# Kernel optimization log

Hardware: AMD Instinct MI355X
Metric: run time of the kernel (lower is better)

The kernel has to match this reference:

```python
import jax, jax.numpy as jnp
import numpy as np

EPS = 1e-5
NUM_GROUPS = 16


def _deform_conv(x, offset, mask, weight):
    """Modulated deformable conv v2, 3x3, stride 1, pad 1, no bias.
    x: [B,C,H,W], offset: [B,18,H,W] (y,x interleaved per kernel point),
    mask: [B,9,H,W], weight: [O,C,3,3].
    """
    B, C, H, W = x.shape
    O = weight.shape[0]
    K = 9
    off = offset.reshape(B, K, 2, H, W)
    dy, dx = off[:, :, 0], off[:, :, 1]  # [B,K,H,W]
    # base sampling grid: output pixel + kernel tap offset (pad=1 -> taps -1..1)
    ky, kx = jnp.meshgrid(jnp.arange(3), jnp.arange(3), indexing='ij')
    ky = (ky.reshape(K) - 1).astype(x.dtype)
    kx = (kx.reshape(K) - 1).astype(x.dtype)
    iy = jnp.arange(H, dtype=x.dtype)[:, None]
    ix = jnp.arange(W, dtype=x.dtype)[None, :]
    py = iy[None, None] + ky[None, :, None, None] + dy  # [B,K,H,W]
    px = ix[None, None] + kx[None, :, None, None] + dx

    y0 = jnp.floor(py)
    x0 = jnp.floor(px)
    wy = py - y0  # grad flows to offsets via these weights
    wx = px - x0

    xf = x.reshape(B, C, H * W)

    def gather(yc, xc, w):
        # yc,xc,w: [B,K,H,W] float; returns weighted samples [B,C,K,H,W]
        valid = (yc >= 0) & (yc <= H - 1) & (xc >= 0) & (xc <= W - 1)
        yi = jnp.clip(yc, 0, H - 1).astype(jnp.int32)
        xi = jnp.clip(xc, 0, W - 1).astype(jnp.int32)
        idx = (yi * W + xi).reshape(B, K * H * W)
        g = jax.vmap(lambda xb, ib: xb[:, ib])(xf, idx)  # [B,C,K*H*W]
        g = g.reshape(B, C, K, H, W)
        wv = (w * valid.astype(x.dtype))[:, None]  # [B,1,K,H,W]
        return g * wv

    val = gather(y0, x0, (1 - wy) * (1 - wx))
    val = val + gather(y0, x0 + 1, (1 - wy) * wx)
    val = val + gather(y0 + 1, x0, wy * (1 - wx))
    val = val + gather(y0 + 1, x0 + 1, wy * wx)

    val = val * mask[:, None]  # modulation: [B,C,K,H,W] * [B,1,K,H,W]
    w = weight.reshape(O, C, K)
    return jnp.einsum('bckhw,ock->bohw', val, w)


def _group_norm(y, gamma, beta):
    B, O, H, W = y.shape
    g = y.reshape(B, NUM_GROUPS, O // NUM_GROUPS, H, W)
    mean = g.mean(axis=(2, 3, 4), keepdims=True)
    var = ((g - mean) ** 2).mean(axis=(2, 3, 4), keepdims=True)
    g = (g - mean) * jax.lax.rsqrt(var + EPS)
    y = g.reshape(B, O, H, W)
    return y * gamma[None, :, None, None] + beta[None, :, None, None]


def setup_inputs() -> dict:
    key = jax.random.key(0)
    k1, k2, k3, k4 = jax.random.split(key, 4)
    B, C, O, H, W = 8, 256, 256, 64, 64
    x = jax.random.normal(k1, (B, C, H, W), jnp.float32)
    offset = jax.random.normal(k2, (B, 18, H, W), jnp.float32)
    mask = jax.random.uniform(k3, (B, 9, H, W), jnp.float32)
    weight = jax.random.normal(k4, (O, C, 3, 3), jnp.float32) * 0.02
    gamma = jnp.ones((O,), jnp.float32)
    beta = jnp.zeros((O,), jnp.float32)
    return {"x": x, "offset": offset, "mask": mask, "weight": weight,
            "gamma": gamma, "beta": beta}


def reference(x, offset, mask, weight, gamma, beta):
    y = _deform_conv(x, offset, mask, weight)
    return _group_norm(y, gamma, beta)
```

## Files before the change

kernel.cpp:

```cpp
#include <hip/hip_runtime.h>
#include <hip/hip_fp16.h>
#include <math.h>

#define BB 8
#define CC 256
#define OO 256
#define HH 64
#define WW 64
#define KK 9
#define HWSZ 4096
#define CKSZ 2304
#define NG 16
#define OPG 16
#define EPSV 1e-5f

typedef _Float16 f16;
typedef f16 f16x8 __attribute__((ext_vector_type(8)));
typedef float f32x4 __attribute__((ext_vector_type(4)));

#define XH_ELEMS ((size_t)BB*HWSZ*CC)
#define WF_ELEMS ((size_t)OO*CKSZ)
#define CV_ELEMS ((size_t)BB*OO*HWSZ)
#define NSTRIP 32

__global__ __launch_bounds__(256) void x_transpose_k(
    const float* __restrict__ x, __half* __restrict__ xh)
{
  int blk = blockIdx.x;
  int b = blk >> 8; int rem = blk & 255;
  int c0 = (rem >> 6) * 64; int hw0 = (rem & 63) * 64;
  __shared__ float st[64][65];
  int t = threadIdx.x;
  #pragma unroll
  for (int i = 0; i < 16; ++i) {
    int idx = t + i*256; int c = idx >> 6, w = idx & 63;
    st[c][w] = x[((size_t)(b*CC + c0 + c))*HWSZ + hw0 + w];
  }
  __syncthreads();
  #pragma unroll
  for (int i = 0; i < 8; ++i) {
    int idx = t + i*256; int r = idx >> 5, cp = idx & 31;
    __half2 v = __floats2half2_rn(st[cp*2][r], st[cp*2+1][r]);
    *(__half2*)&xh[((size_t)(b*HWSZ) + hw0 + r)*CC + c0 + cp*2] = v;
  }
}

__global__ __launch_bounds__(256) void w_frag_k(
    const float* __restrict__ w, __half* __restrict__ wf)
{
  int i = blockIdx.x*256 + threadIdx.x;
  int e = i & 7, lane = (i >> 3) & 63, mi = (i >> 9) & 3;
  int ks = (i >> 11) & 1, wm = (i >> 12) & 3, cc = i >> 14;
  int k = cc >> 2, c0i = cc & 3;
  int o = wm*64 + mi*16 + (lane & 15);
  int c = c0i*64 + ks*32 + (lane >> 4)*8 + e;
  wf[i] = __float2half(w[(o*CC + c)*KK + k]);
}

template<int F16OUT>
__global__ __launch_bounds__(512, 2) void dcn_mfma_k(
    const float* __restrict__ off, const float* __restrict__ msk,
    const __half* __restrict__ xh, const __half* __restrict__ wf,
    float* __restrict__ out32, __half* __restrict__ conv16,
    float* __restrict__ psum)
{
  __shared__ __half sVl[4][128*64];

  const int t = threadIdx.x;
  const int b = blockIdx.x & 7;
  const int strip = blockIdx.x >> 3;
  const int h0 = strip * 2;

  const int lane = t & 63, wid = t >> 6;
  const int lr = lane & 15, lh = lane >> 4;
  const int gp = t >> 2, gq = t & 3;

  auto load_A = [&](int cc, f16x8 a[2][2]) {
    #pragma unroll
    for (int ks = 0; ks < 2; ++ks)
      #pragma unroll
      for (int mi = 0; mi < 2; ++mi) {
        int omi = wid*2 + mi;
        const __half* ap = wf + (size_t)(cc*4 + (omi >> 2))*4096
                              + (size_t)(ks*4 + (omi & 3))*512 + lane*8;
        a[ks][mi] = *(const f16x8*)ap;
      }
  };

  f16x8 aregA[2][2], aregB[2][2];
  load_A(0, aregA);
  load_A(1, aregB);

  f32x4 acc[2][8];
  #pragma unroll
  for (int mi = 0; mi < 2; ++mi)
    #pragma unroll
    for (int ni = 0; ni < 8; ++ni) acc[mi][ni] = (f32x4){0.f,0.f,0.f,0.f};

  const char* xbase = (const char*)xh + (size_t)b * (HWSZ*CC*2);

  uint toff[4]; __half2 twv[4];
  auto compute_taps = [&](int k) {
    int h = h0 + (gp >> 6), w = gp & 63;
    float dy = off[(((b*18) + 2*k    )*HH + h)*WW + w];
    float dx = off[(((b*18) + 2*k + 1)*HH + h)*WW + w];
    float m  = msk[(((b*KK) + k)*HH + h)*WW + w];
    float py = (float)(h + (k/3) - 1) + dy;
    float px = (float)(w + (k%3) - 1) + dx;
    float y0f = floorf(py), x0f = floorf(px);
    float wy = py - y0f, wx = px - x0f;
    int y0 = (int)y0f, x0 = (int)x0f;
    #pragma unroll
    for (int tap = 0; tap < 4; ++tap) {
      int yy = y0 + (tap >> 1), xx = x0 + (tap & 1);
      bool v = (yy >= 0) & (yy < HH) & (xx >= 0) & (xx < WW);
      float bw = ((tap >> 1) ? wy : 1.f - wy) * ((tap & 1) ? wx : 1.f - wx);
      float wgt = v ? bw * m : 0.f;
      int cy = min(max(yy, 0), HH-1), cx = min(max(xx, 0), WW-1);
      toff[tap] = (uint)((cy*WW + cx) * (CC*2));
      twv[tap]  = __float2half2_rn(wgt);
    }
  };
  int tk = 0;
  compute_taps(0);

  auto combine_write = [&](uint4 r0, uint4 r1, uint4 r2, uint4 r3,
                           int oct, __half* dst) {
    const __half2* t0 = (const __half2*)&r0; const __half2* t1 = (const __half2*)&r1;
    const __half2* t2 = (const __half2*)&r2; const __half2* t3 = (const __half2*)&r3;
    __half2 o_[4];
    #pragma unroll
    for (int r = 0; r < 4; ++r)
      o_[r] = __hfma2(twv[0], t0[r], __hfma2(twv[1], t1[r],
              __hfma2(twv[2], t2[r], __hmul2(twv[3], t3[r]))));
    *(uint4*)&dst[gp*64 + ((oct ^ (gp & 7)) << 3)] = *(uint4*)o_;
  };

  auto gather_chunk = [&](int cc, __half* dst) {
    int kn = cc >> 2, c0n = (cc & 3) << 6;
    if (kn != tk) { compute_taps(kn); tk = kn; }
    const char* cb = xbase + (size_t)(c0n*2) + gq*16;
    uint4 a0 = *(const uint4*)(cb + toff[0]);
    uint4 a1 = *(const uint4*)(cb + toff[1]);
    uint4 a2 = *(const uint4*)(cb + toff[2]);
    uint4 a3 = *(const uint4*)(cb + toff[3]);
    uint4 b0 = *(const uint4*)(cb + toff[0] + 64);
    uint4 b1 = *(const uint4*)(cb + toff[1] + 64);
    uint4 b2 = *(const uint4*)(cb + toff[2] + 64);
    uint4 b3 = *(const uint4*)(cb + toff[3] + 64);
    combine_write(a0, a1, a2, a3, gq,     dst);
    combine_write(b0, b1, b2, b3, gq + 4, dst);
  };

  gather_chunk(0, sVl[0]);
  gather_chunk(1, sVl[1]);

  auto do_half = [&](int ccm, int ccf, f16x8 aCur[2][2]) {
    bool pf = (ccf < 36);
    int kn = ccf >> 2, c0n = (ccf & 3) << 6;
    uint4 ga0, ga1, ga2, ga3, gb0, gb1, gb2, gb3;
    if (pf) {
      if (kn != tk) { compute_taps(kn); tk = kn; }
      const char* cb = xbase + (size_t)(c0n*2) + gq*16;
      ga0 = *(const uint4*)(cb + toff[0]);
      ga1 = *(const uint4*)(cb + toff[1]);
      ga2 = *(const uint4*)(cb + toff[2]);
      ga3 = *(const uint4*)(cb + toff[3]);
      gb0 = *(const uint4*)(cb + toff[0] + 64);
      gb1 = *(const uint4*)(cb + toff[1] + 64);
      gb2 = *(const uint4*)(cb + toff[2] + 64);
      gb3 = *(const uint4*)(cb + toff[3] + 64);
    }

    const __half* vb = sVl[ccm & 3];
    #pragma unroll
    for (int ks = 0; ks < 2; ++ks) {
      f16x8 brg[8];
      #pragma unroll
      for (int ni = 0; ni < 8; ++ni) {
        int r = ni*16 + lr;
        brg[ni] = *(const f16x8*)&vb[r*64 + (((ks*4 + lh) ^ (r & 7)) << 3)];
      }
      #pragma unroll
      for (int mi = 0; mi < 2; ++mi)
        #pragma unroll
        for (int ni = 0; ni < 8; ++ni)
          acc[mi][ni] = __builtin_amdgcn_mfma_f32_16x16x32_f16(
              aCur[ks][mi], brg[ni], acc[mi][ni], 0, 0, 0);
    }

    if (pf) {
      __half* dst = sVl[ccf & 3];
      combine_write(ga0, ga1, ga2, ga3, gq,     dst);
      combine_write(gb0, gb1, gb2, gb3, gq + 4, dst);
      load_A(ccf, aCur);
    }
  };

  #pragma unroll 1
  for (int ccp = 0; ccp < 36; ccp += 2) {
    __syncthreads();
    do_half(ccp,     ccp + 2, aregA);
    do_half(ccp + 1, ccp + 3, aregB);
  }

  #pragma unroll
  for (int mi = 0; mi < 2; ++mi) {
    #pragma unroll
    for (int ni = 0; ni < 8; ++ni) {
      int ob = wid*32 + mi*16 + lh*4;
      int pp = ni*16 + lr;
      #pragma unroll
      for (int j = 0; j < 4; ++j) {
        size_t idx = ((size_t)(b*OO + ob + j))*HWSZ + strip*128 + pp;
        if (F16OUT) conv16[idx] = __float2half(acc[mi][ni][j]);
        else        out32[idx] = acc[mi][ni][j];
      }
    }
  }

  if (F16OUT) {
    #pragma unroll
    for (int mi = 0; mi < 2; ++mi) {
      float s1 = 0.f, s2 = 0.f;
      #pragma unroll
      for (int ni = 0; ni < 8; ++ni)
        #pragma unroll
        for (int j = 0; j < 4; ++j) {
          float v = acc[mi][ni][j];
          s1 += v; s2 += v*v;
        }
      #pragma unroll
      for (int d = 32; d > 0; d >>= 1) {
        s1 += __shfl_xor(s1, d);
        s2 += __shfl_xor(s2, d);
      }
      if (lane == 0) {
        int g = wid*2 + mi;
        psum[(size_t)blockIdx.x*32 + g*2]     = s1;
        psum[(size_t)blockIdx.x*32 + g*2 + 1] = s2;
      }
    }
  }
}

__global__ __launch_bounds__(256) void gn_norm2_k(
    const __half* __restrict__ conv16, const float* __restrict__ psum,
    const float* __restrict__ gamma, const float* __restrict__ beta,
    float* __restrict__ out)
{
  int bid = blockIdx.x;
  int bo = bid >> 1;
  int b = bo >> 8, o = bo & 255;
  int g = o >> 4;
  float s1 = 0.f, s2 = 0.f;
  for (int st = 0; st < NSTRIP; ++st) {
    s1 += psum[(size_t)(st*8 + b)*32 + g*2];
    s2 += psum[(size_t)(st*8 + b)*32 + g*2 + 1];
  }
  const float invN = 1.f / (float)(OPG*HWSZ);
  float mean = s1 * invN;
  float var  = s2 * invN - mean*mean;
  float inv = rsqrtf(var + EPSV);
  float sc = gamma[o]*inv;
  float sh = beta[o] - mean*sc;

  size_t e0 = ((size_t)(b*OO + o))*HWSZ + (size_t)(bid & 1)*2048
            + (size_t)threadIdx.x*8;
  uint4 u = *(const uint4*)(conv16 + e0);
  const __half2* hh = (const __half2*)&u;
  float r[8];
  #pragma unroll
  for (int j = 0; j < 4; ++j) {
    float2 f = __half22float2(hh[j]);
    r[2*j] = f.x; r[2*j+1] = f.y;
  }
  *(float4*)&out[e0]     = make_float4(r[0]*sc+sh, r[1]*sc+sh, r[2]*sc+sh, r[3]*sc+sh);
  *(float4*)&out[e0 + 4] = make_float4(r[4]*sc+sh, r[5]*sc+sh, r[6]*sc+sh, r[7]*sc+sh);
}

__global__ __launch_bounds__(1024) void gn_stats_k(
    const float* __restrict__ out, float* __restrict__ stats)
{
  int bg = blockIdx.x;
  const float4* p = (const float4*)(out + (size_t)bg*OPG*HWSZ);
  const int n4 = OPG*HWSZ/4;
  float s1 = 0.f, s2 = 0.f;
  for (int i = threadIdx.x; i < n4; i += 1024) {
    float4 v = p[i];
    s1 += v.x + v.y + v.z + v.w;
    s2 += v.x*v.x + v.y*v.y + v.z*v.z + v.w*v.w;
  }
  #pragma unroll
  for (int o2 = 32; o2 > 0; o2 >>= 1) {
    s1 += __shfl_down(s1, o2);
    s2 += __shfl_down(s2, o2);
  }
  __shared__ float r1[16], r2[16];
  int wd = threadIdx.x >> 6, lane = threadIdx.x & 63;
  if (lane == 0) { r1[wd] = s1; r2[wd] = s2; }
  __syncthreads();
  if (threadIdx.x == 0) {
    float t1 = 0.f, t2 = 0.f;
    #pragma unroll
    for (int i = 0; i < 16; i++) { t1 += r1[i]; t2 += r2[i]; }
    const float invN = 1.f / (float)(OPG*HWSZ);
    float mean = t1 * invN;
    float var  = t2 * invN - mean*mean;
    stats[bg*2]   = mean;
    stats[bg*2+1] = var;
  }
}

__global__ __launch_bounds__(256) void gn_norm_k(
    float* __restrict__ out, const float* __restrict__ stats,
    const float* __restrict__ gamma, const float* __restrict__ beta)
{
  size_t i = (size_t)blockIdx.x*256 + threadIdx.x;
  const size_t n4 = (size_t)BB*OO*HWSZ/4;
  if (i >= n4) return;
  size_t base = i*4;
  int bo = (int)(base / HWSZ);
  int b = bo / OO, o = bo - b*OO;
  int g = o >> 4;
  float mean = stats[(b*NG+g)*2], var = stats[(b*NG+g)*2+1];
  float inv = rsqrtf(var + EPSV);
  float sc = gamma[o]*inv;
  float sh = beta[o] - mean*sc;
  float4 v = *(float4*)&out[base];
  v.x = v.x*sc + sh; v.y = v.y*sc + sh;
  v.z = v.z*sc + sh; v.w = v.w*sc + sh;
  *(float4*)&out[base] = v;
}

extern "C" void kernel_launch(void* const* d_in, const int* in_sizes, int n_in,
                              void* d_out, int out_size, void* d_ws, size_t ws_size,
                              hipStream_t stream) {
  const float* x      = (const float*)d_in[0];
  const float* offset = (const float*)d_in[1];
  const float* mask   = (const float*)d_in[2];
  const float* weight = (const float*)d_in[3];
  const float* gamma  = (const float*)d_in[4];
  const float* beta   = (const float*)d_in[5];
  float* out = (float*)d_out;

  __half* xh   = (__half*)d_ws;
  __half* wf   = xh + XH_ELEMS;
  __half* cv   = wf + WF_ELEMS;
  float* psum  = (float*)(cv + CV_ELEMS);

  const size_t need = (XH_ELEMS + WF_ELEMS + CV_ELEMS)*2
                    + (size_t)BB*NSTRIP*32*4 + 1024;

  x_transpose_k<<<BB*4*64, 256, 0, stream>>>(x, xh);
  w_frag_k<<<(int)(WF_ELEMS/256), 256, 0, stream>>>(weight, wf);

  if (ws_size >= need) {
    dcn_mfma_k<1><<<BB*NSTRIP, 512, 0, stream>>>(offset, mask, xh, wf,
                                                 (float*)nullptr, cv, psum);
    gn_norm2_k<<<4096, 256, 0, stream>>>(cv, psum, gamma, beta, out);
  } else {
    float* stats = (float*)(wf + WF_ELEMS);
    dcn_mfma_k<0><<<BB*NSTRIP, 512, 0, stream>>>(offset, mask, xh, wf,
                                                 out, (__half*)nullptr,
                                                 (float*)nullptr);
    gn_stats_k<<<BB*NG, 1024, 0, stream>>>(out, stats);
    gn_norm_k<<<(int)((size_t)BB*OO*HWSZ/4 + 255)/256, 256, 0, stream>>>(
        out, stats, gamma, beta);
  }
}
```

Measured before the change: 79.97 us.

## Double block size to 1024 threads, one 16-row M tile per wave

The DCN MFMA kernel now launches 1024 threads per block (16 waves) instead of 512. Each wave owns a single 16-output-channel M tile instead of two, so the accumulator and A-fragment registers are halved. Each gather thread handles one 16-byte channel octet instead of two, which cuts per-thread loads and live registers. The aim is more waves in flight to hide gather latency, at the cost of each wave rereading the same B fragments from LDS, which doubles total LDS read traffic per MFMA.

```diff
diff --git a/kernel.cpp b/kernel.cpp
--- a/kernel.cpp
+++ b/kernel.cpp
@@ -58,7 +58,7 @@
 }
 
 template<int F16OUT>
-__global__ __launch_bounds__(512, 2) void dcn_mfma_k(
+__global__ __launch_bounds__(1024, 4) void dcn_mfma_k(
     const float* __restrict__ off, const float* __restrict__ msk,
     const __half* __restrict__ xh, const __half* __restrict__ wf,
     float* __restrict__ out32, __half* __restrict__ conv16,
@@ -73,29 +73,24 @@
 
   const int lane = t & 63, wid = t >> 6;
   const int lr = lane & 15, lh = lane >> 4;
-  const int gp = t >> 2, gq = t & 3;
-
-  auto load_A = [&](int cc, f16x8 a[2][2]) {
-    #pragma unroll
-    for (int ks = 0; ks < 2; ++ks)
-      #pragma unroll
-      for (int mi = 0; mi < 2; ++mi) {
-        int omi = wid*2 + mi;
-        const __half* ap = wf + (size_t)(cc*4 + (omi >> 2))*4096
-                              + (size_t)(ks*4 + (omi & 3))*512 + lane*8;
-        a[ks][mi] = *(const f16x8*)ap;
-      }
-  };
-
-  f16x8 aregA[2][2], aregB[2][2];
+  const int gp = t >> 3, goct = t & 7;
+
+  auto load_A = [&](int cc, f16x8 a[2]) {
+    #pragma unroll
+    for (int ks = 0; ks < 2; ++ks) {
+      const __half* ap = wf + (size_t)(cc*4 + (wid >> 2))*4096
+                            + (size_t)(ks*4 + (wid & 3))*512 + lane*8;
+      a[ks] = *(const f16x8*)ap;
+    }
+  };
+
+  f16x8 aregA[2], aregB[2];
   load_A(0, aregA);
   load_A(1, aregB);
 
-  f32x4 acc[2][8];
-  #pragma unroll
-  for (int mi = 0; mi < 2; ++mi)
-    #pragma unroll
-    for (int ni = 0; ni < 8; ++ni) acc[mi][ni] = (f32x4){0.f,0.f,0.f,0.f};
+  f32x4 acc[8];
+  #pragma unroll
+  for (int ni = 0; ni < 8; ++ni) acc[ni] = (f32x4){0.f,0.f,0.f,0.f};
 
   const char* xbase = (const char*)xh + (size_t)b * (HWSZ*CC*2);
 
@@ -125,7 +120,7 @@
   compute_taps(0);
 
   auto combine_write = [&](uint4 r0, uint4 r1, uint4 r2, uint4 r3,
-                           int oct, __half* dst) {
+                           __half* dst) {
     const __half2* t0 = (const __half2*)&r0; const __half2* t1 = (const __half2*)&r1;
     const __half2* t2 = (const __half2*)&r2; const __half2* t3 = (const __half2*)&r3;
     __half2 o_[4];
@@ -133,43 +128,34 @@
     for (int r = 0; r < 4; ++r)
       o_[r] = __hfma2(twv[0], t0[r], __hfma2(twv[1], t1[r],
               __hfma2(twv[2], t2[r], __hmul2(twv[3], t3[r]))));
-    *(uint4*)&dst[gp*64 + ((oct ^ (gp & 7)) << 3)] = *(uint4*)o_;
+    *(uint4*)&dst[gp*64 + ((goct ^ (gp & 7)) << 3)] = *(uint4*)o_;
   };
 
   auto gather_chunk = [&](int cc, __half* dst) {
     int kn = cc >> 2, c0n = (cc & 3) << 6;
     if (kn != tk) { compute_taps(kn); tk = kn; }
-    const char* cb = xbase + (size_t)(c0n*2) + gq*16;
-    uint4 a0 = *(const uint4*)(cb + toff[0]);
-    uint4 a1 = *(const uint4*)(cb + toff[1]);
-    uint4 a2 = *(const uint4*)(cb + toff[2]);
-    uint4 a3 = *(const uint4*)(cb + toff[3]);
-    uint4 b0 = *(const uint4*)(cb + toff[0] + 64);
-    uint4 b1 = *(const uint4*)(cb + toff[1] + 64);
-    uint4 b2 = *(const uint4*)(cb + toff[2] + 64);
-    uint4 b3 = *(const uint4*)(cb + toff[3] + 64);
-    combine_write(a0, a1, a2, a3, gq,     dst);
-    combine_write(b0, b1, b2, b3, gq + 4, dst);
+    const char* cb = xbase + (size_t)(c0n*2) + goct*16;
+    uint4 r0 = *(const uint4*)(cb + toff[0]);
+    uint4 r1 = *(const uint4*)(cb + toff[1]);
+    uint4 r2 = *(const uint4*)(cb + toff[2]);
+    uint4 r3 = *(const uint4*)(cb + toff[3]);
+    combine_write(r0, r1, r2, r3, dst);
   };
 
   gather_chunk(0, sVl[0]);
   gather_chunk(1, sVl[1]);
 
-  auto do_half = [&](int ccm, int ccf, f16x8 aCur[2][2]) {
+  auto do_half = [&](int ccm, int ccf, f16x8 aCur[2]) {
     bool pf = (ccf < 36);
     int kn = ccf >> 2, c0n = (ccf & 3) << 6;
-    uint4 ga0, ga1, ga2, ga3, gb0, gb1, gb2, gb3;
+    uint4 g0, g1, g2, g3;
     if (pf) {
       if (kn != tk) { compute_taps(kn); tk = kn; }
-      const char* cb = xbase + (size_t)(c0n*2) + gq*16;
-      ga0 = *(const uint4*)(cb + toff[0]);
-      ga1 = *(const uint4*)(cb + toff[1]);
-      ga2 = *(const uint4*)(cb + toff[2]);
-      ga3 = *(const uint4*)(cb + toff[3]);
-      gb0 = *(const uint4*)(cb + toff[0] + 64);
-      gb1 = *(const uint4*)(cb + toff[1] + 64);
-      gb2 = *(const uint4*)(cb + toff[2] + 64);
-      gb3 = *(const uint4*)(cb + toff[3] + 64);
+      const char* cb = xbase + (size_t)(c0n*2) + goct*16;
+      g0 = *(const uint4*)(cb + toff[0]);
+      g1 = *(const uint4*)(cb + toff[1]);
+      g2 = *(const uint4*)(cb + toff[2]);
+      g3 = *(const uint4*)(cb + toff[3]);
     }
 
     const __half* vb = sVl[ccm & 3];
@@ -182,17 +168,13 @@
         brg[ni] = *(const f16x8*)&vb[r*64 + (((ks*4 + lh) ^ (r & 7)) << 3)];
       }
       #pragma unroll
-      for (int mi = 0; mi < 2; ++mi)
-        #pragma unroll
-        for (int ni = 0; ni < 8; ++ni)
-          acc[mi][ni] = __builtin_amdgcn_mfma_f32_16x16x32_f16(
-              aCur[ks][mi], brg[ni], acc[mi][ni], 0, 0, 0);
+      for (int ni = 0; ni < 8; ++ni)
+        acc[ni] = __builtin_amdgcn_mfma_f32_16x16x32_f16(
+            aCur[ks], brg[ni], acc[ni], 0, 0, 0);
     }
 
     if (pf) {
-      __half* dst = sVl[ccf & 3];
-      combine_write(ga0, ga1, ga2, ga3, gq,     dst);
-      combine_write(gb0, gb1, gb2, gb3, gq + 4, dst);
+      combine_write(g0, g1, g2, g3, sVl[ccf & 3]);
       load_A(ccf, aCur);
     }
   };
@@ -205,41 +187,34 @@
   }
 
   #pragma unroll
-  for (int mi = 0; mi < 2; ++mi) {
-    #pragma unroll
-    for (int ni = 0; ni < 8; ++ni) {
-      int ob = wid*32 + mi*16 + lh*4;
-      int pp = ni*16 + lr;
+  for (int ni = 0; ni < 8; ++ni) {
+    int pp = ni*16 + lr;
+    #pragma unroll
+    for (int j = 0; j < 4; ++j) {
+      int o = wid*16 + lh*4 + j;
+      size_t idx = ((size_t)(b*OO + o))*HWSZ + strip*128 + pp;
+      if (F16OUT) conv16[idx] = __float2half(acc[ni][j]);
+      else        out32[idx] = acc[ni][j];
+    }
+  }
+
+  if (F16OUT) {
+    float s1 = 0.f, s2 = 0.f;
+    #pragma unroll
+    for (int ni = 0; ni < 8; ++ni)
       #pragma unroll
       for (int j = 0; j < 4; ++j) {
-        size_t idx = ((size_t)(b*OO + ob + j))*HWSZ + strip*128 + pp;
-        if (F16OUT) conv16[idx] = __float2half(acc[mi][ni][j]);
-        else        out32[idx] = acc[mi][ni][j];
+        float v = acc[ni][j];
+        s1 += v; s2 += v*v;
       }
-    }
-  }
-
-  if (F16OUT) {
-    #pragma unroll
-    for (int mi = 0; mi < 2; ++mi) {
-      float s1 = 0.f, s2 = 0.f;
-      #pragma unroll
-      for (int ni = 0; ni < 8; ++ni)
-        #pragma unroll
-        for (int j = 0; j < 4; ++j) {
-          float v = acc[mi][ni][j];
-          s1 += v; s2 += v*v;
-        }
-      #pragma unroll
-      for (int d = 32; d > 0; d >>= 1) {
-        s1 += __shfl_xor(s1, d);
-        s2 += __shfl_xor(s2, d);
-      }
-      if (lane == 0) {
-        int g = wid*2 + mi;
-        psum[(size_t)blockIdx.x*32 + g*2]     = s1;
-        psum[(size_t)blockIdx.x*32 + g*2 + 1] = s2;
-      }
+    #pragma unroll
+    for (int d = 32; d > 0; d >>= 1) {
+      s1 += __shfl_xor(s1, d);
+      s2 += __shfl_xor(s2, d);
+    }
+    if (lane == 0) {
+      psum[(size_t)blockIdx.x*32 + wid*2]     = s1;
+      psum[(size_t)blockIdx.x*32 + wid*2 + 1] = s2;
     }
   }
 }
@@ -356,14 +331,14 @@
   w_frag_k<<<(int)(WF_ELEMS/256), 256, 0, stream>>>(weight, wf);
 
   if (ws_size >= need) {
-    dcn_mfma_k<1><<<BB*NSTRIP, 512, 0, stream>>>(offset, mask, xh, wf,
-                                                 (float*)nullptr, cv, psum);
+    dcn_mfma_k<1><<<BB*NSTRIP, 1024, 0, stream>>>(offset, mask, xh, wf,
+                                                  (float*)nullptr, cv, psum);
     gn_norm2_k<<<4096, 256, 0, stream>>>(cv, psum, gamma, beta, out);
   } else {
     float* stats = (float*)(wf + WF_ELEMS);
-    dcn_mfma_k<0><<<BB*NSTRIP, 512, 0, stream>>>(offset, mask, xh, wf,
-                                                 out, (__half*)nullptr,
-                                                 (float*)nullptr);
+    dcn_mfma_k<0><<<BB*NSTRIP, 1024, 0, stream>>>(offset, mask, xh, wf,
+                                                  out, (__half*)nullptr,
+                                                  (float*)nullptr);
     gn_stats_k<<<BB*NG, 1024, 0, stream>>>(out, stats);
     gn_norm_k<<<(int)((size_t)BB*OO*HWSZ/4 + 255)/256, 256, 0, stream>>>(
         out, stats, gamma, beta);
```

Result: slower. 83.10 us (+3.9%).
